# Optimization experiments

Hardware: AMD Instinct MI355X
Metric: run time of the kernel (lower is better)

Reference implementation:

```python
import jax, jax.numpy as jnp
import numpy as np

NEG_SLOPE = 0.01  # torch leaky_relu default

N_NODES = 100000
N_EDGES = 1600000
D = 64
N_BBOX = 4096


def setup_inputs() -> dict:
    key = jax.random.key(0)
    ks = jax.random.split(key, 9)
    x = jax.random.normal(ks[0], (N_NODES, D), dtype=jnp.float32)
    edge_index = jax.random.randint(ks[1], (2, N_EDGES), 0, N_NODES, dtype=jnp.int64)
    bbox = jax.random.randint(ks[2], (N_BBOX,), 0, N_NODES, dtype=jnp.int64)
    s = 1.0 / np.sqrt(D)
    W1_rel = jax.random.normal(ks[3], (D, D), dtype=jnp.float32) * s
    b1 = jax.random.normal(ks[4], (D,), dtype=jnp.float32) * s
    W1_root = jax.random.normal(ks[5], (D, D), dtype=jnp.float32) * s
    W2_rel = jax.random.normal(ks[6], (D, D), dtype=jnp.float32) * s
    b2 = jax.random.normal(ks[7], (D,), dtype=jnp.float32) * s
    W2_root = jax.random.normal(ks[8], (D, D), dtype=jnp.float32) * s
    return {"x": x, "edge_index": edge_index, "bbox": bbox,
            "W1_rel": W1_rel, "b1": b1, "W1_root": W1_root,
            "W2_rel": W2_rel, "b2": b2, "W2_root": W2_root}


def graph_conv(x, src, dst, W_rel, b, W_root):
    # PyG GraphConv: out_i = W_rel @ (sum_{j in N(i)} x_j) + b + W_root @ x_i
    msg = x[src]                                        # [E, D] gather
    agg = jax.ops.segment_sum(msg, dst, num_segments=x.shape[0])  # [N, D] scatter-add
    return agg @ W_rel + b + x @ W_root


def reference(x, edge_index, bbox, W1_rel, b1, W1_root, W2_rel, b2, W2_root):
    src, dst = edge_index[0], edge_index[1]
    h = graph_conv(x, src, dst, W1_rel, b1, W1_root)
    h = jax.nn.leaky_relu(h, NEG_SLOPE)
    # dropout is identity at inference (training=False)
    h = graph_conv(h, src, dst, W2_rel, b2, W2_root)
    h = jax.nn.leaky_relu(h, NEG_SLOPE)
    return h[bbox]
```

## Files before the change

kernel.cpp:

```cpp
#include <hip/hip_runtime.h>

#define N_NODES 100000
#define N_EDGES 1600000
#define D 64
#define N_BBOX 4096
#define CAP 64
#define NBITW 3136
#define SLICE 12500
#define NBLK_A 6250
#define SEGCAP 96
#define NTILE1 (N_NODES / 16)
#define NTILE2 (N_BBOX / 16)

typedef short bf16x8 __attribute__((ext_vector_type(8)));
typedef float f32x4 __attribute__((ext_vector_type(4)));

__device__ __forceinline__ int bperm(int srclane, int v) {
  return __builtin_amdgcn_ds_bpermute(srclane << 2, v);
}
__device__ __forceinline__ float lrelu(float v) {
  return fmaxf(v, 0.01f * v);
}
__device__ __forceinline__ bool testbit(const unsigned* bits, int i) {
  return (bits[i >> 5] >> (i & 31)) & 1u;
}
__device__ __forceinline__ short f2bf(float f) {
  unsigned u = __float_as_uint(f);
  u += 0x7FFFu + ((u >> 16) & 1u);
  return (short)(u >> 16);
}

__global__ __launch_bounds__(256) void prep_kernel(const float4* __restrict__ x4,
                                                   bf16x8* __restrict__ xb,
                                                   const int* __restrict__ bbox,
                                                   unsigned* __restrict__ is_bbox_bits,
                                                   unsigned* __restrict__ needed_bits,
                                                   int* __restrict__ cnt) {
  const int i = blockIdx.x * 256 + threadIdx.x;
  if (i < N_NODES) cnt[i] = 0;
  if (i < N_NODES * 8) {
    const float4 a = x4[i * 2], b = x4[i * 2 + 1];
    bf16x8 r;
    r[0] = f2bf(a.x); r[1] = f2bf(a.y); r[2] = f2bf(a.z); r[3] = f2bf(a.w);
    r[4] = f2bf(b.x); r[5] = f2bf(b.y); r[6] = f2bf(b.z); r[7] = f2bf(b.w);
    xb[i] = r;
  } else {
    const int t = i - N_NODES * 8;
    if (t < N_BBOX) {
      const int n = bbox[t];
      const unsigned m = 1u << (n & 31);
      atomicOr(&is_bbox_bits[n >> 5], m);
      atomicOr(&needed_bits[n >> 5], m);
    }
  }
}

__global__ __launch_bounds__(256) void scan_kernel(const int* __restrict__ src,
                                                   const int* __restrict__ dst,
                                                   const unsigned* __restrict__ is_bbox_bits,
                                                   unsigned* __restrict__ needed_bits,
                                                   int* __restrict__ qcnt,
                                                   int* __restrict__ qseg) {
  __shared__ int lcnt[8];
  __shared__ int lbuf[8 * SEGCAP];
  const int t = threadIdx.x;
  const int lane = t & 63;
  const int e = blockIdx.x * 256 + t;
  if (t < 8) lcnt[t] = 0;
  __syncthreads();

  const int d = dst[e];
  const int s = src[e];
  if (testbit(is_bbox_bits, d)) {
    atomicOr(&needed_bits[s >> 5], 1u << (s & 31));
  }
  const int q = d / SLICE;
  const int pv = s | ((d - q * SLICE) << 17);
#pragma unroll
  for (int qq = 0; qq < 8; qq++) {
    const unsigned long long mask = __ballot(q == qq);
    if (!mask) continue;
    const int nq = __popcll(mask);
    const int leader = (int)__builtin_ctzll(mask);
    int base = 0;
    if (lane == leader) base = atomicAdd(&lcnt[qq], nq);
    base = __builtin_amdgcn_readlane(base, leader);
    if (q == qq) {
      const int p = base + __popcll(mask & ((1ull << lane) - 1ull));
      if (p < SEGCAP) lbuf[qq * SEGCAP + p] = pv;
    }
  }
  __syncthreads();

  const size_t segbase = (size_t)blockIdx.x * 8;
  if (t < 8) qcnt[segbase + t] = (lcnt[t] > SEGCAP) ? SEGCAP : lcnt[t];
  for (int i = t; i < 8 * SEGCAP; i += 256) {
    const int q2 = i / SEGCAP, p2 = i - q2 * SEGCAP;
    if (p2 < lcnt[q2]) qseg[(segbase + q2) * SEGCAP + p2] = lbuf[i];
  }
}

__global__ __launch_bounds__(256) void scatterB_kernel(const int* __restrict__ qcnt,
                                                       const int* __restrict__ qseg,
                                                       const unsigned* __restrict__ needed_bits,
                                                       int* __restrict__ cnt,
                                                       int* __restrict__ slots) {
  const int sl = blockIdx.x & 7;
  const int bidx = blockIdx.x >> 3;
  const int nblk = gridDim.x >> 3;
  const int base_node = sl * SLICE;
  const int sub = threadIdx.x >> 4;
  const int pp = threadIdx.x & 15;

  for (int b0 = bidx * 16; b0 < NBLK_A; b0 += nblk * 16) {
    const int b = b0 + sub;
    if (b >= NBLK_A) continue;
    const int n = qcnt[(size_t)b * 8 + sl];
    const int* seg = qseg + ((size_t)b * 8 + sl) * SEGCAP;
    for (int p = pp; p < n; p += 16) {
      const int pv = seg[p];
      const int d = base_node + (pv >> 17);
      if (!testbit(needed_bits, d)) continue;
      const int pos = atomicAdd(&cnt[d], 1);
      if (pos < CAP) slots[(size_t)d * CAP + pos] = pv & 0x1FFFF;
    }
  }
}

__device__ __forceinline__ void gather_rows(const uint4* __restrict__ rows,
                                            const int* __restrict__ slots,
                                            int node, int n, int lane,
                                            float accf[8]) {
  const int g = lane >> 3, c = lane & 7;
  const int myslot = (lane < n) ? slots[(size_t)node * CAP + lane] : 0;
#pragma unroll
  for (int i = 0; i < 8; i++) accf[i] = 0.f;
  for (int e0 = 0; e0 < n; e0 += 64) {
    int idx[8], s[8];
    uint4 v[8];
#pragma unroll
    for (int u = 0; u < 8; u++) {
      idx[u] = e0 + u * 8 + g;
      s[u] = bperm(idx[u], myslot);
    }
#pragma unroll
    for (int u = 0; u < 8; u++) {
      v[u] = make_uint4(0u, 0u, 0u, 0u);
      if (idx[u] < n) v[u] = rows[(size_t)s[u] * 8 + c];
    }
#pragma unroll
    for (int u = 0; u < 8; u++) {
      accf[0] += __uint_as_float(v[u].x << 16);
      accf[1] += __uint_as_float(v[u].x & 0xFFFF0000u);
      accf[2] += __uint_as_float(v[u].y << 16);
      accf[3] += __uint_as_float(v[u].y & 0xFFFF0000u);
      accf[4] += __uint_as_float(v[u].z << 16);
      accf[5] += __uint_as_float(v[u].z & 0xFFFF0000u);
      accf[6] += __uint_as_float(v[u].w << 16);
      accf[7] += __uint_as_float(v[u].w & 0xFFFF0000u);
    }
  }
#pragma unroll
  for (int off = 8; off < 64; off <<= 1)
#pragma unroll
    for (int i = 0; i < 8; i++) accf[i] += __shfl_xor(accf[i], off);
}

__global__ __launch_bounds__(256) void gd1_kernel(
    const uint4* __restrict__ xb4, const short* __restrict__ xb,
    const unsigned* __restrict__ needed_bits, const int* __restrict__ cnt,
    const int* __restrict__ slots, const float* __restrict__ W1rel,
    const float* __restrict__ b1, const float* __restrict__ W1root,
    short* __restrict__ hb) {
  __shared__ __align__(16) short aggt[16][72];
  const int t = threadIdx.x;
  const int lane = t & 63;
  const int wid = t >> 6;
  const int cn = lane & 15, quad = lane >> 4;

  bf16x8 brel[2], broot[2];
#pragma unroll
  for (int kh = 0; kh < 2; kh++)
#pragma unroll
    for (int i = 0; i < 8; i++) {
      const int k = kh * 32 + quad * 8 + i;
      brel[kh][i] = f2bf(W1rel[k * D + wid * 16 + cn]);
      broot[kh][i] = f2bf(W1root[k * D + wid * 16 + cn]);
    }
  const float bj = b1[wid * 16 + cn];

  for (int tile = blockIdx.x; tile < NTILE1; tile += gridDim.x) {
    const int node0 = tile * 16;
#pragma unroll
    for (int r4 = 0; r4 < 4; r4++) {
      const int row = wid * 4 + r4;
      const int node = node0 + row;
      int n = cnt[node];
      n = (n > CAP) ? CAP : n;
      if (n == 0) {
        if (lane < 8) {
          bf16x8 z = {0, 0, 0, 0, 0, 0, 0, 0};
          *(bf16x8*)(&aggt[row][lane * 8]) = z;
        }
        continue;
      }
      float accf[8];
      gather_rows(xb4, slots, node, n, lane, accf);
      if (lane < 8) {
        bf16x8 r;
#pragma unroll
        for (int i = 0; i < 8; i++) r[i] = f2bf(accf[i]);
        *(bf16x8*)(&aggt[row][lane * 8]) = r;
      }
    }
    __syncthreads();
    const int mrow = node0 + cn;
    const bool ndrow = testbit(needed_bits, mrow);
    f32x4 acc = {};
#pragma unroll
    for (int kh = 0; kh < 2; kh++) {
      const bf16x8 a_agg = *(const bf16x8*)(&aggt[cn][kh * 32 + quad * 8]);
      bf16x8 a_x = {0, 0, 0, 0, 0, 0, 0, 0};
      if (ndrow)
        a_x = *(const bf16x8*)(xb + (size_t)mrow * D + kh * 32 + quad * 8);
      acc = __builtin_amdgcn_mfma_f32_16x16x32_bf16(a_agg, brel[kh], acc, 0, 0, 0);
      acc = __builtin_amdgcn_mfma_f32_16x16x32_bf16(a_x, broot[kh], acc, 0, 0, 0);
    }
#pragma unroll
    for (int r = 0; r < 4; r++) {
      const int row = quad * 4 + r;
      if (testbit(needed_bits, node0 + row))
        hb[(size_t)(node0 + row) * D + wid * 16 + cn] = f2bf(lrelu(acc[r] + bj));
    }
    __syncthreads();
  }
}

__global__ __launch_bounds__(256) void gd2_kernel(
    const uint4* __restrict__ hb4, const short* __restrict__ hb,
    const int* __restrict__ cnt, const int* __restrict__ slots,
    const int* __restrict__ bbox, const float* __restrict__ W2rel,
    const float* __restrict__ b2, const float* __restrict__ W2root,
    float* __restrict__ out) {
  __shared__ __align__(16) short aggt[16][72];
  __shared__ int nodes_s[16];
  const int t = threadIdx.x;
  const int lane = t & 63;
  const int wid = t >> 6;
  const int cn = lane & 15, quad = lane >> 4;
  const int t0 = blockIdx.x * 16;

  if (t < 16) nodes_s[t] = bbox[t0 + t];

  bf16x8 brel[2], broot[2];
#pragma unroll
  for (int kh = 0; kh < 2; kh++)
#pragma unroll
    for (int i = 0; i < 8; i++) {
      const int k = kh * 32 + quad * 8 + i;
      brel[kh][i] = f2bf(W2rel[k * D + wid * 16 + cn]);
      broot[kh][i] = f2bf(W2root[k * D + wid * 16 + cn]);
    }
  const float bj = b2[wid * 16 + cn];
  __syncthreads();

#pragma unroll
  for (int r4 = 0; r4 < 4; r4++) {
    const int row = wid * 4 + r4;
    const int node = nodes_s[row];
    int n = cnt[node];
    n = (n > CAP) ? CAP : n;
    if (n == 0) {
      if (lane < 8) {
        bf16x8 z = {0, 0, 0, 0, 0, 0, 0, 0};
        *(bf16x8*)(&aggt[row][lane * 8]) = z;
      }
      continue;
    }
    float accf[8];
    gather_rows(hb4, slots, node, n, lane, accf);
    if (lane < 8) {
      bf16x8 r;
#pragma unroll
      for (int i = 0; i < 8; i++) r[i] = f2bf(accf[i]);
      *(bf16x8*)(&aggt[row][lane * 8]) = r;
    }
  }
  __syncthreads();

  const int rnode = nodes_s[cn];
  f32x4 acc = {};
#pragma unroll
  for (int kh = 0; kh < 2; kh++) {
    const bf16x8 a_agg = *(const bf16x8*)(&aggt[cn][kh * 32 + quad * 8]);
    const bf16x8 a_h = *(const bf16x8*)(hb + (size_t)rnode * D + kh * 32 + quad * 8);
    acc = __builtin_amdgcn_mfma_f32_16x16x32_bf16(a_agg, brel[kh], acc, 0, 0, 0);
    acc = __builtin_amdgcn_mfma_f32_16x16x32_bf16(a_h, broot[kh], acc, 0, 0, 0);
  }
#pragma unroll
  for (int r = 0; r < 4; r++) {
    const int row = quad * 4 + r;
    out[(size_t)(t0 + row) * D + wid * 16 + cn] = lrelu(acc[r] + bj);
  }
}


extern "C" void kernel_launch(void* const* d_in, const int* in_sizes, int n_in,
                              void* d_out, int out_size, void* d_ws, size_t ws_size,
                              hipStream_t stream) {
  const float* x = (const float*)d_in[0];
  const int* ei = (const int*)d_in[1];
  const int* src = ei;
  const int* dst = ei + N_EDGES;
  const int* bbox = (const int*)d_in[2];
  const float* W1rel = (const float*)d_in[3];
  const float* b1 = (const float*)d_in[4];
  const float* W1root = (const float*)d_in[5];
  const float* W2rel = (const float*)d_in[6];
  const float* b2 = (const float*)d_in[7];
  const float* W2root = (const float*)d_in[8];
  float* out = (float*)d_out;

  char* ws = (char*)d_ws;
  size_t off = 0;
  auto alloc = [&](size_t bytes) -> char* {
    char* p = ws + off;
    off = (off + bytes + 511) & ~(size_t)511;
    return p;
  };
  unsigned* is_bbox_bits = (unsigned*)alloc(NBITW * sizeof(unsigned));
  unsigned* needed_bits = (unsigned*)alloc(NBITW * sizeof(unsigned));
  char* zero_end = ws + off;
  int* cnt = (int*)alloc(N_NODES * sizeof(int));
  int* qcnt = (int*)alloc((size_t)NBLK_A * 8 * sizeof(int));
  int* qseg = (int*)alloc((size_t)NBLK_A * 8 * SEGCAP * sizeof(int));
  int* slots = (int*)alloc((size_t)N_NODES * CAP * sizeof(int));
  short* xb = (short*)alloc((size_t)N_NODES * D * sizeof(short));
  short* hb = (short*)alloc((size_t)N_NODES * D * sizeof(short));

  hipMemsetAsync(is_bbox_bits, 0, (size_t)(zero_end - (char*)is_bbox_bits), stream);
  prep_kernel<<<(N_NODES * 8 + N_BBOX + 255) / 256, 256, 0, stream>>>(
      (const float4*)x, (bf16x8*)xb, bbox, is_bbox_bits, needed_bits, cnt);
  scan_kernel<<<NBLK_A, 256, 0, stream>>>(src, dst, is_bbox_bits, needed_bits,
                                          qcnt, qseg);
  scatterB_kernel<<<2048, 256, 0, stream>>>(qcnt, qseg, needed_bits, cnt, slots);
  gd1_kernel<<<2048, 256, 0, stream>>>((const uint4*)xb, xb, needed_bits, cnt,
                                       slots, W1rel, b1, W1root, hb);
  gd2_kernel<<<NTILE2, 256, 0, stream>>>((const uint4*)hb, hb, cnt, slots, bbox,
                                         W2rel, b2, W2root, out);
}
```

Before: 201.1 us.

## Pre-swizzle bf16 weights in prep, shrink gather chunks, give each gd1 block two tiles

The prep kernel now converts all four weight matrices once into a bf16 MFMA-fragment layout, so gd1 and gd2 each load their B fragments with vector loads instead of strided fp32 loads and per-element conversion in every block. The gather loop steps through 32 edges at a time with guards, so low-degree nodes issue fewer wasted permutes and loads. gd1 switches from a grid-stride loop to a fixed two tiles per block, with one barrier between all gathers and the MFMA stage. This launches far more blocks (3125 instead of 2048) and spends more shared memory per block.

Measured after the change: 194.7 us. -3.2%, faster.

```diff
diff --git a/kernel.cpp b/kernel.cpp
--- a/kernel.cpp
+++ b/kernel.cpp
@@ -11,6 +11,7 @@
 #define SEGCAP 96
 #define NTILE1 (N_NODES / 16)
 #define NTILE2 (N_BBOX / 16)
+#define TPB1 2
 
 typedef short bf16x8 __attribute__((ext_vector_type(8)));
 typedef float f32x4 __attribute__((ext_vector_type(4)));
@@ -35,7 +36,12 @@
                                                    const int* __restrict__ bbox,
                                                    unsigned* __restrict__ is_bbox_bits,
                                                    unsigned* __restrict__ needed_bits,
-                                                   int* __restrict__ cnt) {
+                                                   int* __restrict__ cnt,
+                                                   const float* __restrict__ W1rel,
+                                                   const float* __restrict__ W1root,
+                                                   const float* __restrict__ W2rel,
+                                                   const float* __restrict__ W2root,
+                                                   short* __restrict__ wf) {
   const int i = blockIdx.x * 256 + threadIdx.x;
   if (i < N_NODES) cnt[i] = 0;
   if (i < N_NODES * 8) {
@@ -51,6 +57,17 @@
       const unsigned m = 1u << (n & 31);
       atomicOr(&is_bbox_bits[n >> 5], m);
       atomicOr(&needed_bits[n >> 5], m);
+    } else if (t < N_BBOX + 4 * 4096) {
+      const int t2 = t - N_BBOX;
+      const int layer = t2 >> 13;
+      const int r = t2 & 8191;
+      const int m = r >> 12;
+      const int e = r & 4095;
+      const int kh = e >> 11, quad = (e >> 9) & 3;
+      const int col = (e >> 3) & 63, ii = e & 7;
+      const int k = kh * 32 + quad * 8 + ii;
+      const float* W = layer ? (m ? W2root : W2rel) : (m ? W1root : W1rel);
+      wf[t2] = f2bf(W[k * 64 + col]);
     }
   }
 }
@@ -135,30 +152,34 @@
   const int myslot = (lane < n) ? slots[(size_t)node * CAP + lane] : 0;
 #pragma unroll
   for (int i = 0; i < 8; i++) accf[i] = 0.f;
-  for (int e0 = 0; e0 < n; e0 += 64) {
-    int idx[8], s[8];
-    uint4 v[8];
-#pragma unroll
-    for (int u = 0; u < 8; u++) {
-      idx[u] = e0 + u * 8 + g;
-      s[u] = bperm(idx[u], myslot);
-    }
-#pragma unroll
-    for (int u = 0; u < 8; u++) {
-      v[u] = make_uint4(0u, 0u, 0u, 0u);
-      if (idx[u] < n) v[u] = rows[(size_t)s[u] * 8 + c];
-    }
-#pragma unroll
-    for (int u = 0; u < 8; u++) {
-      accf[0] += __uint_as_float(v[u].x << 16);
-      accf[1] += __uint_as_float(v[u].x & 0xFFFF0000u);
-      accf[2] += __uint_as_float(v[u].y << 16);
-      accf[3] += __uint_as_float(v[u].y & 0xFFFF0000u);
-      accf[4] += __uint_as_float(v[u].z << 16);
-      accf[5] += __uint_as_float(v[u].z & 0xFFFF0000u);
-      accf[6] += __uint_as_float(v[u].w << 16);
-      accf[7] += __uint_as_float(v[u].w & 0xFFFF0000u);
-    }
+  for (int e0 = 0; e0 < n; e0 += 32) {
+    const int rem = n - e0;
+    int idx[4], s[4];
+    uint4 v[4];
+#pragma unroll
+    for (int u = 0; u < 4; u++)
+      if (u * 8 < rem) {
+        idx[u] = e0 + u * 8 + g;
+        s[u] = bperm(idx[u], myslot);
+      }
+#pragma unroll
+    for (int u = 0; u < 4; u++)
+      if (u * 8 < rem) {
+        v[u] = make_uint4(0u, 0u, 0u, 0u);
+        if (idx[u] < n) v[u] = rows[(size_t)s[u] * 8 + c];
+      }
+#pragma unroll
+    for (int u = 0; u < 4; u++)
+      if (u * 8 < rem) {
+        accf[0] += __uint_as_float(v[u].x << 16);
+        accf[1] += __uint_as_float(v[u].x & 0xFFFF0000u);
+        accf[2] += __uint_as_float(v[u].y << 16);
+        accf[3] += __uint_as_float(v[u].y & 0xFFFF0000u);
+        accf[4] += __uint_as_float(v[u].z << 16);
+        accf[5] += __uint_as_float(v[u].z & 0xFFFF0000u);
+        accf[6] += __uint_as_float(v[u].w << 16);
+        accf[7] += __uint_as_float(v[u].w & 0xFFFF0000u);
+      }
   }
 #pragma unroll
   for (int off = 8; off < 64; off <<= 1)
@@ -169,28 +190,29 @@
 __global__ __launch_bounds__(256) void gd1_kernel(
     const uint4* __restrict__ xb4, const short* __restrict__ xb,
     const unsigned* __restrict__ needed_bits, const int* __restrict__ cnt,
-    const int* __restrict__ slots, const float* __restrict__ W1rel,
-    const float* __restrict__ b1, const float* __restrict__ W1root,
-    short* __restrict__ hb) {
-  __shared__ __align__(16) short aggt[16][72];
+    const int* __restrict__ slots, const short* __restrict__ wf1,
+    const float* __restrict__ b1, short* __restrict__ hb) {
+  __shared__ __align__(16) short aggt[TPB1][16][72];
   const int t = threadIdx.x;
   const int lane = t & 63;
   const int wid = t >> 6;
   const int cn = lane & 15, quad = lane >> 4;
-
+  const int col = wid * 16 + cn;
+
+  const bf16x8* wfv = (const bf16x8*)wf1;
   bf16x8 brel[2], broot[2];
 #pragma unroll
-  for (int kh = 0; kh < 2; kh++)
-#pragma unroll
-    for (int i = 0; i < 8; i++) {
-      const int k = kh * 32 + quad * 8 + i;
-      brel[kh][i] = f2bf(W1rel[k * D + wid * 16 + cn]);
-      broot[kh][i] = f2bf(W1root[k * D + wid * 16 + cn]);
-    }
-  const float bj = b1[wid * 16 + cn];
-
-  for (int tile = blockIdx.x; tile < NTILE1; tile += gridDim.x) {
-    const int node0 = tile * 16;
+  for (int kh = 0; kh < 2; kh++) {
+    brel[kh] = wfv[(kh * 4 + quad) * 64 + col];
+    broot[kh] = wfv[((2 + kh) * 4 + quad) * 64 + col];
+  }
+  const float bj = b1[col];
+
+  const int tile0 = blockIdx.x * TPB1;
+  const int ntt = (NTILE1 - tile0 < TPB1) ? (NTILE1 - tile0) : TPB1;
+
+  for (int tt = 0; tt < ntt; tt++) {
+    const int node0 = (tile0 + tt) * 16;
 #pragma unroll
     for (int r4 = 0; r4 < 4; r4++) {
       const int row = wid * 4 + r4;
@@ -200,7 +222,7 @@
       if (n == 0) {
         if (lane < 8) {
           bf16x8 z = {0, 0, 0, 0, 0, 0, 0, 0};
-          *(bf16x8*)(&aggt[row][lane * 8]) = z;
+          *(bf16x8*)(&aggt[tt][row][lane * 8]) = z;
         }
         continue;
       }
@@ -210,16 +232,20 @@
         bf16x8 r;
 #pragma unroll
         for (int i = 0; i < 8; i++) r[i] = f2bf(accf[i]);
-        *(bf16x8*)(&aggt[row][lane * 8]) = r;
-      }
-    }
-    __syncthreads();
+        *(bf16x8*)(&aggt[tt][row][lane * 8]) = r;
+      }
+    }
+  }
+  __syncthreads();
+
+  for (int tt = 0; tt < ntt; tt++) {
+    const int node0 = (tile0 + tt) * 16;
     const int mrow = node0 + cn;
     const bool ndrow = testbit(needed_bits, mrow);
     f32x4 acc = {};
 #pragma unroll
     for (int kh = 0; kh < 2; kh++) {
-      const bf16x8 a_agg = *(const bf16x8*)(&aggt[cn][kh * 32 + quad * 8]);
+      const bf16x8 a_agg = *(const bf16x8*)(&aggt[tt][cn][kh * 32 + quad * 8]);
       bf16x8 a_x = {0, 0, 0, 0, 0, 0, 0, 0};
       if (ndrow)
         a_x = *(const bf16x8*)(xb + (size_t)mrow * D + kh * 32 + quad * 8);
@@ -230,38 +256,35 @@
     for (int r = 0; r < 4; r++) {
       const int row = quad * 4 + r;
       if (testbit(needed_bits, node0 + row))
-        hb[(size_t)(node0 + row) * D + wid * 16 + cn] = f2bf(lrelu(acc[r] + bj));
-    }
-    __syncthreads();
+        hb[(size_t)(node0 + row) * D + col] = f2bf(lrelu(acc[r] + bj));
+    }
   }
 }
 
 __global__ __launch_bounds__(256) void gd2_kernel(
     const uint4* __restrict__ hb4, const short* __restrict__ hb,
     const int* __restrict__ cnt, const int* __restrict__ slots,
-    const int* __restrict__ bbox, const float* __restrict__ W2rel,
-    const float* __restrict__ b2, const float* __restrict__ W2root,
-    float* __restrict__ out) {
+    const int* __restrict__ bbox, const short* __restrict__ wf2,
+    const float* __restrict__ b2, float* __restrict__ out) {
   __shared__ __align__(16) short aggt[16][72];
   __shared__ int nodes_s[16];
   const int t = threadIdx.x;
   const int lane = t & 63;
   const int wid = t >> 6;
   const int cn = lane & 15, quad = lane >> 4;
+  const int col = wid * 16 + cn;
   const int t0 = blockIdx.x * 16;
 
   if (t < 16) nodes_s[t] = bbox[t0 + t];
 
+  const bf16x8* wfv = (const bf16x8*)wf2;
   bf16x8 brel[2], broot[2];
 #pragma unroll
-  for (int kh = 0; kh < 2; kh++)
-#pragma unroll
-    for (int i = 0; i < 8; i++) {
-      const int k = kh * 32 + quad * 8 + i;
-      brel[kh][i] = f2bf(W2rel[k * D + wid * 16 + cn]);
-      broot[kh][i] = f2bf(W2root[k * D + wid * 16 + cn]);
-    }
-  const float bj = b2[wid * 16 + cn];
+  for (int kh = 0; kh < 2; kh++) {
+    brel[kh] = wfv[(kh * 4 + quad) * 64 + col];
+    broot[kh] = wfv[((2 + kh) * 4 + quad) * 64 + col];
+  }
+  const float bj = b2[col];
   __syncthreads();
 
 #pragma unroll
@@ -300,7 +323,7 @@
 #pragma unroll
   for (int r = 0; r < 4; r++) {
     const int row = quad * 4 + r;
-    out[(size_t)(t0 + row) * D + wid * 16 + cn] = lrelu(acc[r] + bj);
+    out[(size_t)(t0 + row) * D + col] = lrelu(acc[r] + bj);
   }
 }
 
@@ -337,15 +360,17 @@
   int* slots = (int*)alloc((size_t)N_NODES * CAP * sizeof(int));
   short* xb = (short*)alloc((size_t)N_NODES * D * sizeof(short));
   short* hb = (short*)alloc((size_t)N_NODES * D * sizeof(short));
+  short* wf = (short*)alloc((size_t)4 * 4096 * sizeof(short));
 
   hipMemsetAsync(is_bbox_bits, 0, (size_t)(zero_end - (char*)is_bbox_bits), stream);
-  prep_kernel<<<(N_NODES * 8 + N_BBOX + 255) / 256, 256, 0, stream>>>(
-      (const float4*)x, (bf16x8*)xb, bbox, is_bbox_bits, needed_bits, cnt);
+  prep_kernel<<<(N_NODES * 8 + N_BBOX + 4 * 4096 + 255) / 256, 256, 0, stream>>>(
+      (const float4*)x, (bf16x8*)xb, bbox, is_bbox_bits, needed_bits, cnt,
+      W1rel, W1root, W2rel, W2root, wf);
   scan_kernel<<<NBLK_A, 256, 0, stream>>>(src, dst, is_bbox_bits, needed_bits,
                                           qcnt, qseg);
   scatterB_kernel<<<2048, 256, 0, stream>>>(qcnt, qseg, needed_bits, cnt, slots);
-  gd1_kernel<<<2048, 256, 0, stream>>>((const uint4*)xb, xb, needed_bits, cnt,
-                                       slots, W1rel, b1, W1root, hb);
+  gd1_kernel<<<(NTILE1 + TPB1 - 1) / TPB1, 256, 0, stream>>>(
+      (const uint4*)xb, xb, needed_bits, cnt, slots, wf, b1, hb);
   gd2_kernel<<<NTILE2, 256, 0, stream>>>((const uint4*)hb, hb, cnt, slots, bbox,
-                                         W2rel, b2, W2root, out);
-}
+                                         wf + 8192, b2, out);
+}
```
